# Kernel tuning notes

Hardware: AMD Instinct MI355X
Metric: run time of the kernel (lower is better)

The kernel has to match this reference:

```python
import jax, jax.numpy as jnp
import numpy as np

SNR_DB = 20.0   # fixed draw from snr_range=(20, 20)
B_COEF = 0.02   # pink-noise IIR coefficient


def setup_inputs() -> dict:
    key = jax.random.key(0)
    k1, k2 = jax.random.split(key)
    L = 16_777_216  # 2**24 audio samples
    audio = jax.random.normal(k1, (L,), dtype=jnp.float32)
    white = jax.random.normal(k2, (L,), dtype=jnp.float32)  # driving white noise for pink branch
    return {"audio": audio, "white": white}


def _pink_noise(white):
    # p[0] = 0; p[i] = B*w[i] + (1-B)*p[i-1]  -> linear recurrence x_i = a_i*x_{i-1} + u_i
    b = jnp.asarray(B_COEF, white.dtype)
    a = jnp.full(white.shape, 1.0 - B_COEF, white.dtype).at[0].set(0.0)
    u = (b * white).at[0].set(0.0)

    def combine(lhs, rhs):
        a1, u1 = lhs
        a2, u2 = rhs
        return a1 * a2, a2 * u1 + u2

    _, pink = jax.lax.associative_scan(combine, (a, u))
    return pink


def reference(audio, white):
    signal_power = jnp.mean(audio ** 2)
    noise_power = signal_power / (10.0 ** (SNR_DB / 10.0))
    noise = _pink_noise(white) * jnp.sqrt(noise_power)
    return audio + noise
```

## Files before the change

kernel.cpp:

```cpp
#include <hip/hip_runtime.h>
#include <math.h>

#define L_TOTAL (1 << 24)

constexpr float A_COEF = 0.98f;
constexpr float B_COEF = 0.02f;

constexpr int T    = 256;
constexpr int S    = 16;
constexpr int TS   = T * S;
constexpr int WARM = 512;

__global__ __launch_bounds__(256) void sumsq_kernel(const float4* __restrict__ a4,
                                                    double* __restrict__ acc,
                                                    int n4) {
    int idx    = blockIdx.x * blockDim.x + threadIdx.x;
    int stride = gridDim.x * blockDim.x;
    float s = 0.f;
    for (int i = idx; i < n4; i += stride) {
        float4 v = a4[i];
        s += v.x * v.x + v.y * v.y + v.z * v.z + v.w * v.w;
    }
    #pragma unroll
    for (int o = 32; o > 0; o >>= 1) s += __shfl_down(s, o, 64);
    __shared__ float wsum[4];
    int lane = threadIdx.x & 63;
    int wv   = threadIdx.x >> 6;
    if (lane == 0) wsum[wv] = s;
    __syncthreads();
    if (threadIdx.x == 0) {
        float b = wsum[0] + wsum[1] + wsum[2] + wsum[3];
        atomicAdd(acc, (double)b);
    }
}

__global__ __launch_bounds__(256) void pink_add_kernel(const float* __restrict__ audio,
                                                       const float* __restrict__ white,
                                                       const double* __restrict__ acc,
                                                       float* __restrict__ out) {
    const float scale = (float)sqrt((*acc) * (1.0 / ((double)L_TOTAL * 100.0)));

    __shared__ float lds[TS + TS / 16];
    __shared__ float wave_tot[4];
    __shared__ float wsum[4];

    const int tid  = threadIdx.x;
    const int lane = tid & 63;
    const int wv   = tid >> 6;
    const int base = blockIdx.x * TS;

    const float4* ap = reinterpret_cast<const float4*>(audio + base);
    float4 av[4];
    #pragma unroll
    for (int q = 0; q < 4; ++q) av[q] = ap[q * T + tid];

    const float4* wp = reinterpret_cast<const float4*>(white + base + tid * S);
    float w[S];
    #pragma unroll
    for (int q = 0; q < S / 4; ++q) {
        float4 v = wp[q];
        w[4 * q + 0] = v.x; w[4 * q + 1] = v.y;
        w[4 * q + 2] = v.z; w[4 * q + 3] = v.w;
    }

    float2 wu = make_float2(0.f, 0.f);
    if (blockIdx.x > 0) {
        const float2* up = reinterpret_cast<const float2*>(white + base - WARM);
        wu = up[tid];
    }

    const float a2 = A_COEF * A_COEF;
    const float a4 = a2 * a2;
    const float a8 = a4 * a4;
    const float beta = a8 * a8;
    const float b2 = beta * beta, b4 = b2 * b2, b8 = b4 * b4;
    const float b16 = b8 * b8, b32 = b16 * b16, b64 = b32 * b32;
    const float bpow[6] = {beta, b2, b4, b8, b16, b32};

    const float beta_l = exp2f((float)lane * log2f(beta));
    float b64w = 1.f;
    #pragma unroll
    for (int i = 0; i < 3; ++i) if (wv > i) b64w *= b64;
    const float beta_t = beta_l * b64w;

    #pragma unroll
    for (int j = 0; j < S; ++j) w[j] *= B_COEF;
    if (base == 0 && tid == 0) w[0] = 0.f;

    float p = 0.f;
    #pragma unroll
    for (int j = 0; j < S; ++j) p = fmaf(A_COEF, p, w[j]);

    float W = p;
    #pragma unroll
    for (int i = 0; i < 6; ++i) {
        const int o = 1 << i;
        float up = __shfl_up(W, o, 64);
        if (lane >= o) W = fmaf(bpow[i], up, W);
    }

    float part = fmaf(A_COEF, B_COEF * wu.x, B_COEF * wu.y);
    part *= exp2f((float)(255 - tid) * log2f(a2));
    #pragma unroll
    for (int o = 32; o > 0; o >>= 1) part += __shfl_down(part, o, 64);

    if (lane == 63) wave_tot[wv] = W;
    if (lane == 0)  wsum[wv] = part;
    __syncthreads();

    const float G0 = wave_tot[0], G1 = wave_tot[1];
    const float G2 = wave_tot[2], G3 = wave_tot[3];
    const float P1 = G0;
    const float P2 = fmaf(P1, b64, G1);
    const float P3 = fmaf(P2, b64, G2);
    const float P  = (wv == 0) ? 0.f : (wv == 1) ? P1 : (wv == 2) ? P2 : P3;
    const float Cw = wsum[0] + wsum[1] + wsum[2] + wsum[3];

    const float Wp = __shfl_up(W, 1, 64);
    const float E  = ((lane == 0) ? 0.f : Wp) + P * beta_l;
    const float C  = E + Cw * beta_t;

    float p2 = C;
    const int lb = tid * 17;
    #pragma unroll
    for (int j = 0; j < S; ++j) {
        p2 = fmaf(A_COEF, p2, w[j]);
        lds[lb + j] = p2;
    }
    __syncthreads();

    float4* op = reinterpret_cast<float4*>(out + base);
    #pragma unroll
    for (int q = 0; q < 4; ++q) {
        const int i4 = q * T + tid;
        const int i  = i4 * 4;
        const int pi = i + (i >> 4);
        float4 a = av[q];
        float4 r;
        r.x = fmaf(lds[pi + 0], scale, a.x);
        r.y = fmaf(lds[pi + 1], scale, a.y);
        r.z = fmaf(lds[pi + 2], scale, a.z);
        r.w = fmaf(lds[pi + 3], scale, a.w);
        op[i4] = r;
    }
}

extern "C" void kernel_launch(void* const* d_in, const int* in_sizes, int n_in,
                              void* d_out, int out_size, void* d_ws, size_t ws_size,
                              hipStream_t stream) {
    const float* audio = (const float*)d_in[0];
    const float* white = (const float*)d_in[1];
    float* out         = (float*)d_out;
    double* acc        = (double*)d_ws;

    hipMemsetAsync(d_ws, 0, sizeof(double), stream);

    const int n4 = L_TOTAL / 4;
    sumsq_kernel<<<1024, 256, 0, stream>>>((const float4*)audio, acc, n4);

    const int blocks = L_TOTAL / TS;
    pink_add_kernel<<<blocks, 256, 0, stream>>>(audio, white, acc, out);
}
```

Measured before the change: 179.8 us.

## Replace atomic sum with per-block partials, drop memset, restructure pink scan

The sum-of-squares kernel now writes one float partial per block instead of doing a double atomicAdd, so the memset launch goes away. Each pink_add block re-reduces the 1024 partials itself and computes the scale in float. The local recurrence values are stored and fixed up with precomputed powers of A instead of rerunning the serial recurrence. The audio load is moved after the scan, and __syncthreads is replaced with a raw lgkmcnt wait plus s_barrier. The costs are a redundant 1024-element reduction in every block and a float rather than double accumulation of the power sum.

```diff
diff --git a/kernel.cpp b/kernel.cpp
--- a/kernel.cpp
+++ b/kernel.cpp
@@ -10,9 +10,14 @@
 constexpr int S    = 16;
 constexpr int TS   = T * S;
 constexpr int WARM = 512;
+constexpr int NPART = 1024;
+
+__device__ __forceinline__ void block_sync_lds() {
+    asm volatile("s_waitcnt lgkmcnt(0)\n\ts_barrier" ::: "memory");
+}
 
 __global__ __launch_bounds__(256) void sumsq_kernel(const float4* __restrict__ a4,
-                                                    double* __restrict__ acc,
+                                                    float* __restrict__ partials,
                                                     int n4) {
     int idx    = blockIdx.x * blockDim.x + threadIdx.x;
     int stride = gridDim.x * blockDim.x;
@@ -28,31 +33,23 @@
     int wv   = threadIdx.x >> 6;
     if (lane == 0) wsum[wv] = s;
     __syncthreads();
-    if (threadIdx.x == 0) {
-        float b = wsum[0] + wsum[1] + wsum[2] + wsum[3];
-        atomicAdd(acc, (double)b);
-    }
+    if (threadIdx.x == 0)
+        partials[blockIdx.x] = wsum[0] + wsum[1] + wsum[2] + wsum[3];
 }
 
 __global__ __launch_bounds__(256) void pink_add_kernel(const float* __restrict__ audio,
                                                        const float* __restrict__ white,
-                                                       const double* __restrict__ acc,
+                                                       const float* __restrict__ partials,
                                                        float* __restrict__ out) {
-    const float scale = (float)sqrt((*acc) * (1.0 / ((double)L_TOTAL * 100.0)));
-
     __shared__ float lds[TS + TS / 16];
     __shared__ float wave_tot[4];
     __shared__ float wsum[4];
+    __shared__ float psum[4];
 
     const int tid  = threadIdx.x;
     const int lane = tid & 63;
     const int wv   = tid >> 6;
     const int base = blockIdx.x * TS;
-
-    const float4* ap = reinterpret_cast<const float4*>(audio + base);
-    float4 av[4];
-    #pragma unroll
-    for (int q = 0; q < 4; ++q) av[q] = ap[q * T + tid];
 
     const float4* wp = reinterpret_cast<const float4*>(white + base + tid * S);
     float w[S];
@@ -62,17 +59,18 @@
         w[4 * q + 0] = v.x; w[4 * q + 1] = v.y;
         w[4 * q + 2] = v.z; w[4 * q + 3] = v.w;
     }
-
     float2 wu = make_float2(0.f, 0.f);
     if (blockIdx.x > 0) {
         const float2* up = reinterpret_cast<const float2*>(white + base - WARM);
         wu = up[tid];
     }
+    const float4 pp = reinterpret_cast<const float4*>(partials)[tid];
 
-    const float a2 = A_COEF * A_COEF;
-    const float a4 = a2 * a2;
-    const float a8 = a4 * a4;
-    const float beta = a8 * a8;
+    float apow[S];
+    apow[0] = A_COEF;
+    #pragma unroll
+    for (int j = 1; j < S; ++j) apow[j] = apow[j - 1] * A_COEF;
+    const float beta = apow[S - 1];
     const float b2 = beta * beta, b4 = b2 * b2, b8 = b4 * b4;
     const float b16 = b8 * b8, b32 = b16 * b16, b64 = b32 * b32;
     const float bpow[6] = {beta, b2, b4, b8, b16, b32};
@@ -87,9 +85,10 @@
     for (int j = 0; j < S; ++j) w[j] *= B_COEF;
     if (base == 0 && tid == 0) w[0] = 0.f;
 
+    float l[S];
     float p = 0.f;
     #pragma unroll
-    for (int j = 0; j < S; ++j) p = fmaf(A_COEF, p, w[j]);
+    for (int j = 0; j < S; ++j) { p = fmaf(A_COEF, p, w[j]); l[j] = p; }
 
     float W = p;
     #pragma unroll
@@ -99,14 +98,19 @@
         if (lane >= o) W = fmaf(bpow[i], up, W);
     }
 
+    const float a2c = A_COEF * A_COEF;
     float part = fmaf(A_COEF, B_COEF * wu.x, B_COEF * wu.y);
-    part *= exp2f((float)(255 - tid) * log2f(a2));
+    part *= exp2f((float)(255 - tid) * log2f(a2c));
     #pragma unroll
     for (int o = 32; o > 0; o >>= 1) part += __shfl_down(part, o, 64);
 
+    float ss = pp.x + pp.y + pp.z + pp.w;
+    #pragma unroll
+    for (int o = 32; o > 0; o >>= 1) ss += __shfl_down(ss, o, 64);
+
     if (lane == 63) wave_tot[wv] = W;
-    if (lane == 0)  wsum[wv] = part;
-    __syncthreads();
+    if (lane == 0)  { wsum[wv] = part; psum[wv] = ss; }
+    block_sync_lds();
 
     const float G0 = wave_tot[0], G1 = wave_tot[1];
     const float G2 = wave_tot[2], G3 = wave_tot[3];
@@ -115,19 +119,24 @@
     const float P3 = fmaf(P2, b64, G2);
     const float P  = (wv == 0) ? 0.f : (wv == 1) ? P1 : (wv == 2) ? P2 : P3;
     const float Cw = wsum[0] + wsum[1] + wsum[2] + wsum[3];
+    const float sumsq = psum[0] + psum[1] + psum[2] + psum[3];
+    const float scale = sqrtf(sumsq * (1.0f / ((float)L_TOTAL * 100.0f)));
 
     const float Wp = __shfl_up(W, 1, 64);
     const float E  = ((lane == 0) ? 0.f : Wp) + P * beta_l;
     const float C  = E + Cw * beta_t;
 
-    float p2 = C;
     const int lb = tid * 17;
     #pragma unroll
-    for (int j = 0; j < S; ++j) {
-        p2 = fmaf(A_COEF, p2, w[j]);
-        lds[lb + j] = p2;
-    }
-    __syncthreads();
+    for (int j = 0; j < S; ++j)
+        lds[lb + j] = fmaf(C, apow[j], l[j]);
+
+    const float4* ap = reinterpret_cast<const float4*>(audio + base);
+    float4 av[4];
+    #pragma unroll
+    for (int q = 0; q < 4; ++q) av[q] = ap[q * T + tid];
+
+    block_sync_lds();
 
     float4* op = reinterpret_cast<float4*>(out + base);
     #pragma unroll
@@ -151,13 +160,11 @@
     const float* audio = (const float*)d_in[0];
     const float* white = (const float*)d_in[1];
     float* out         = (float*)d_out;
-    double* acc        = (double*)d_ws;
-
-    hipMemsetAsync(d_ws, 0, sizeof(double), stream);
+    float* partials    = (float*)d_ws;
 
     const int n4 = L_TOTAL / 4;
-    sumsq_kernel<<<1024, 256, 0, stream>>>((const float4*)audio, acc, n4);
+    sumsq_kernel<<<NPART, 256, 0, stream>>>((const float4*)audio, partials, n4);
 
     const int blocks = L_TOTAL / TS;
-    pink_add_kernel<<<blocks, 256, 0, stream>>>(audio, white, acc, out);
+    pink_add_kernel<<<blocks, 256, 0, stream>>>(audio, white, partials, out);
 }
```

After: 171.4 us. -4.7%, faster.
